# Optimization experiments

Measured on AMD Instinct MI355X. Metric: run time of the kernel, lower is better.

## Reference

```python
import jax, jax.numpy as jnp
import numpy as np

N = 50000          # nodes
E = 800000         # edges
F_IN = 128         # in_channels
C = 64             # cell channels
NCELLS = 2
STEPS = 4
MULT = 4
N_EDGE_SLOTS = 14  # 2+3+4+5 mixed-op edges per cell
N_OPS = 8          # switch_on
NUM_CLASSES = 40
BN_EPS = 1e-5
GCNII_ALPHA = 0.1


def setup_inputs() -> dict:
    key = jax.random.key(0)
    ks = jax.random.split(key, 20)
    def w(k, shape, fan_in):
        return jax.random.normal(k, shape, dtype=jnp.float32) / np.float32(np.sqrt(fan_in))
    return {
        "x": jax.random.normal(ks[0], (N, F_IN), dtype=jnp.float32),
        "edge_index": jax.random.randint(ks[1], (2, E), 0, N, dtype=jnp.int32),
        "alphas": 0.001 * jax.random.normal(ks[2], (N_EDGE_SLOTS, N_OPS), dtype=jnp.float32),
        "stem_W": w(ks[3], (F_IN, 3 * C), F_IN),
        "pre_W": w(ks[4], (F_IN, C), F_IN),
        "pre0_W0": w(ks[5], (3 * C, C), 3 * C),
        "pre1_W0": w(ks[6], (3 * C, C), 3 * C),
        "pre0_W1": w(ks[7], (3 * C, C), 3 * C),
        "pre1_W1": w(ks[8], (MULT * C, C), MULT * C),
        "W_gcn": w(ks[9], (NCELLS, N_EDGE_SLOTS, C, C), C),
        "W_sage_self": w(ks[10], (NCELLS, N_EDGE_SLOTS, C, C), C),
        "W_sage_nei": w(ks[11], (NCELLS, N_EDGE_SLOTS, C, C), C),
        "W_gin": w(ks[12], (NCELLS, N_EDGE_SLOTS, C, C), C),
        "W_gc1": w(ks[13], (NCELLS, N_EDGE_SLOTS, C, C), C),
        "W_gc2": w(ks[14], (NCELLS, N_EDGE_SLOTS, C, C), C),
        "W_mlp": w(ks[15], (NCELLS, N_EDGE_SLOTS, C, C), C),
        "W_gcnii": w(ks[16], (NCELLS, N_EDGE_SLOTS, C, C), C),
        "cls_W": w(ks[17], (MULT * C + 1, NUM_CLASSES), MULT * C + 1),
        "cls_b": jnp.zeros((NUM_CLASSES,), dtype=jnp.float32),
    }


def reference(x, edge_index, alphas, stem_W, pre_W, pre0_W0, pre1_W0, pre0_W1, pre1_W1,
              W_gcn, W_sage_self, W_sage_nei, W_gin, W_gc1, W_gc2, W_mlp, W_gcnii,
              cls_W, cls_b):
    src, dst = edge_index[0], edge_index[1]
    deg = jax.ops.segment_sum(jnp.ones((E,), jnp.float32), dst, num_segments=N)
    deg = jnp.maximum(deg, 1.0)
    inv_deg = 1.0 / deg
    inv_sqrt = jax.lax.rsqrt(deg)
    edge_norm = (inv_sqrt[src] * inv_sqrt[dst])[:, None]  # [E,1] sym-normalized coeff

    def bn(h):  # batch norm over node axis, no affine (gamma=1, beta=0)
        m = jnp.mean(h, axis=0)
        v = jnp.var(h, axis=0)
        return (h - m) * jax.lax.rsqrt(v + BN_EPS)

    def mlp(xx, W, act):  # Linear(no bias) -> BN -> optional ReLU
        h = bn(xx @ W)
        return jnp.maximum(h, 0.0) if act else h

    relu = lambda t: jnp.maximum(t, 0.0)

    def mixed_op(h, wv, ci, ej, x0):
        # shared message-passing aggregations of h over edge_index
        msg = h[src]                                             # [E,C] gather
        s_sum = jax.ops.segment_sum(msg, dst, num_segments=N)    # sum agg
        s_mean = s_sum * inv_deg[:, None]                        # mean agg
        s_norm = jax.ops.segment_sum(msg * edge_norm, dst, num_segments=N)  # gcn agg
        out = wv[1] * h                                          # skip_connect (wv[0]: none)
        out = out + wv[2] * relu(s_norm @ W_gcn[ci, ej])
        out = out + wv[3] * (h @ W_sage_self[ci, ej] + s_mean @ W_sage_nei[ci, ej])
        out = out + wv[4] * relu((h + s_sum) @ W_gin[ci, ej])
        out = out + wv[5] * (h @ W_gc1[ci, ej] + s_sum @ W_gc2[ci, ej])
        out = out + wv[6] * relu(h @ W_mlp[ci, ej])
        out = out + wv[7] * relu(((1.0 - GCNII_ALPHA) * s_norm + GCNII_ALPHA * x0) @ W_gcnii[ci, ej])
        return out

    wmix = jax.nn.softmax(alphas, axis=-1)  # [14,8], identical across cells

    s0 = s1 = mlp(x, stem_W, act=False)     # stem: MLP([in, 3C], act=None)
    x0 = mlp(x, pre_W, act=True)            # preprocess: MLP([in, C], relu)
    pre_ws = [(pre0_W0, pre1_W0), (pre0_W1, pre1_W1)]
    for ci in range(NCELLS):
        p0, p1 = pre_ws[ci]
        a = mlp(s0, p0, act=True)
        b = mlp(s1, p1, act=True)
        states = [a, b]
        offset = 0
        for _ in range(STEPS):
            s = None
            for j, h in enumerate(states):
                o = mixed_op(h, wmix[offset + j], ci, offset + j, x0)
                s = o if s is None else s + o
            offset += len(states)
            states.append(s)
        out_cell = jnp.concatenate(states[-MULT:], axis=1)  # [N, 4C]
        s0, s1 = s1, out_cell

    pooled = jnp.mean(s1, axis=1, keepdims=True)            # AdaptiveAvgPool1d(1) over channels
    logits = jnp.concatenate([pooled, s1], axis=1) @ cls_W + cls_b
    return logits
```

## Files before the change

### kernel.cpp

```cpp
#include <hip/hip_runtime.h>
#include <stdint.h>

typedef unsigned short u16;
typedef __attribute__((ext_vector_type(8))) short bh8;
typedef __attribute__((ext_vector_type(4))) float f4;

__device__ __forceinline__ float b2f(u16 u){ union{unsigned u; float f;} x; x.u = ((unsigned)u)<<16; return x.f; }
__device__ __forceinline__ u16 f2b(float f){ union{float f; unsigned u;} x; x.f = f; return (u16)((x.u + 0x7fffu + ((x.u>>16)&1u))>>16); }
__device__ __forceinline__ bh8 ld8(const u16* p){ return *reinterpret_cast<const bh8*>(p); }

#define NBK 512

__global__ __launch_bounds__(256) void k_hist(const int* dst, int* hist, int E){
  __shared__ int h[NBK];
  for (int i=threadIdx.x;i<NBK;i+=256) h[i]=0;
  __syncthreads();
  int stride = 256*gridDim.x;
  for (int i = blockIdx.x*256+threadIdx.x; i<E; i+=stride)
    atomicAdd(&h[dst[i]>>7], 1);
  __syncthreads();
  for (int i=threadIdx.x;i<NBK;i+=256){
    int v=h[i]; if (v) atomicAdd(&hist[i], v);
  }
}

__global__ __launch_bounds__(512) void k_scanb(const int* hist, int* bbase, int* bcursor){
  int t = threadIdx.x, lane = t&63, wv = t>>6;
  __shared__ int ws[8];
  int v = hist[t];
  int x = v;
  #pragma unroll
  for (int o=1;o<64;o<<=1){ int u=__shfl_up(x,(unsigned)o,64); if(lane>=o) x+=u; }
  if (lane==63) ws[wv]=x;
  __syncthreads();
  if (t<8){
    int s=ws[t];
    #pragma unroll
    for (int o=1;o<8;o<<=1){ int u=__shfl_up(s,(unsigned)o,8); if (t>=o) s+=u; }
    ws[t]=s;
  }
  __syncthreads();
  int base = (wv==0)?0:ws[wv-1];
  int ex = base + x - v;
  bbase[t]=ex; bcursor[t]=ex;
  if (t==511) bbase[512]=ex+v;
}

__global__ __launch_bounds__(256) void k_bucket(const int* src, const int* dst,
                                                int* bcursor, unsigned* bkt, int E, int nblk){
  __shared__ int h[NBK], base[NBK], lc[NBK];
  int per = (E + nblk - 1)/nblk;
  int e0 = blockIdx.x*per, e1 = min(E, e0+per);
  for (int i=threadIdx.x;i<NBK;i+=256){ h[i]=0; lc[i]=0; }
  __syncthreads();
  for (int e=e0+threadIdx.x; e<e1; e+=256) atomicAdd(&h[dst[e]>>7], 1);
  __syncthreads();
  for (int i=threadIdx.x;i<NBK;i+=256){
    int c=h[i]; base[i] = c ? atomicAdd(&bcursor[i], c) : 0;
  }
  __syncthreads();
  for (int e=e0+threadIdx.x; e<e1; e+=256){
    int d = dst[e];
    int b = d>>7;
    int r = atomicAdd(&lc[b], 1);
    bkt[base[b]+r] = ((unsigned)(d&127)<<25) | (unsigned)src[e];
  }
}

__global__ __launch_bounds__(128) void k_degb(const unsigned* bkt, const int* bbase,
                                              int* off, float* inv_deg, float* invs,
                                              int N, int E){
  int b = blockIdx.x, t = threadIdx.x;
  __shared__ int cnt[128];
  __shared__ int w0tot;
  cnt[t]=0;
  __syncthreads();
  int e0=bbase[b], e1=bbase[b+1];
  for (int e=e0+t; e<e1; e+=128) atomicAdd(&cnt[bkt[e]>>25], 1);
  __syncthreads();
  int v = cnt[t];
  int lane=t&63, wv=t>>6;
  int x=v;
  #pragma unroll
  for (int o=1;o<64;o<<=1){ int u=__shfl_up(x,(unsigned)o,64); if(lane>=o) x+=u; }
  if (t==63) w0tot=x;
  __syncthreads();
  int ex = x - v + (wv ? w0tot : 0);
  int node = b*128 + t;
  if (node < N){
    off[node] = e0 + ex;
    int d = (v<1)?1:v;
    float df=(float)d;
    inv_deg[node]=1.0f/df;
    invs[node]=rsqrtf(df);
  }
  if (b==0 && t==0) off[N]=E;
}

__global__ __launch_bounds__(128) void k_fillb(const unsigned* bkt, const int* bbase,
                                               const int* off, const float* invs,
                                               int2* csr, int N){
  int b = blockIdx.x, t = threadIdx.x;
  __shared__ int cur[128];
  int node = b*128 + t;
  cur[t] = (node < N) ? off[node] : 0;
  __syncthreads();
  int e0=bbase[b], e1=bbase[b+1];
  for (int e=e0+t; e<e1; e+=128){
    unsigned v = bkt[e];
    int i = (int)(v>>25);
    int s = (int)(v & 0x1FFFFFFu);
    int pos = atomicAdd(&cur[i], 1);
    csr[pos] = make_int2(s, __float_as_int(invs[s]));
  }
}

__global__ void k_softmax(const float* alphas, float* wmix){
  int t = threadIdx.x; int r = t >> 3, o = t & 7;
  if (r < 14){
    float v = alphas[r*8+o];
    float m = v;
    #pragma unroll
    for (int d=1; d<8; d<<=1) m = fmaxf(m, __shfl_xor(m, d, 8));
    float e = expf(v - m);
    float s = e;
    #pragma unroll
    for (int d=1; d<8; d<<=1) s += __shfl_xor(s, d, 8);
    wmix[r*8+o] = e / s;
  }
}

__global__ void k_f2b(const float* a, u16* b, int n){
  int i = blockIdx.x*256 + threadIdx.x;
  if (i < n) b[i] = f2b(a[i]);
}

__global__ void k_pack2d(const float* W, u16* Bp, int K, int ncol){
  int i = blockIdx.x*256 + threadIdx.x;
  if (i < K*ncol){
    int k = i / ncol, n = i - k*ncol;
    Bp[(size_t)n*K + k] = f2b(W[i]);
  }
}

struct PackArgs { const float* W[8]; const float* wmix; u16* dst; };
__global__ void k_pack_ops8(PackArgs P){
  int i = blockIdx.x*256 + threadIdx.x;
  if (i >= 28*8*4096) return;
  int slot28 = i >> 15;
  int rem = i & 32767;
  int mat = rem >> 12;
  int e = rem & 4095;
  int k = e >> 6, n = e & 63;
  const float* wm = P.wmix + (slot28 % 14)*8;
  size_t off = (size_t)slot28*4096 + e;
  float v = 0.f;
  switch(mat){
    case 0: v = wm[2]*P.W[0][off]; break;
    case 1: v = wm[3]*P.W[1][off] + wm[5]*P.W[4][off] + ((k==n) ? wm[1] : 0.f); break;
    case 2: v = wm[3]*P.W[2][off]; break;
    case 3: v = wm[4]*P.W[3][off]; break;
    case 4: v = wm[5]*P.W[5][off]; break;
    case 5: v = wm[6]*P.W[6][off]; break;
    case 6: v = 0.9f*wm[7]*P.W[7][off]; break;
    case 7: v = 0.1f*wm[7]*P.W[7][off]; break;
  }
  P.dst[(((size_t)slot28*8 + mat)<<12) + (n<<6) + (((k>>3) ^ (n&7))<<3) + (k&7)] = f2b(v);
}

__global__ void k_pack_cls(const float* W, u16* Bp){
  int i = blockIdx.x*256 + threadIdx.x;
  if (i < 48*256){
    int n = i >> 8, k = i & 255;
    float v = 0.f;
    if (n < 40) v = W[(size_t)(1+k)*40 + n] + W[n] * (1.f/256.f);
    Bp[(size_t)n*256 + k] = f2b(v);
  }
}

template<int NT>
__global__ __launch_bounds__(256) void k_gemm(const u16* A, int lda, const u16* Bp, int K,
                                              u16* Tb, int ldT, int Nn, float* S){
  __shared__ float sred[4][NT*16][2];
  int tid = threadIdx.x, wv = tid>>6, lane = tid&63, q = lane>>4, t = lane&15;
  int row0 = blockIdx.x*128 + wv*32;
  f4 acc[2][NT];
  #pragma unroll
  for (int a=0;a<2;a++)
    #pragma unroll
    for (int b=0;b<NT;b++) acc[a][b] = (f4){0.f,0.f,0.f,0.f};
  int nkb = K >> 5;
  const u16* arow0 = A + (size_t)(row0 + t)*lda + q*8;
  const u16* arow1 = arow0 + (size_t)16*lda;
  const u16* brow  = Bp + (size_t)t*K + q*8;
  for (int kb = 0; kb < nkb; ++kb){
    bh8 a0 = ld8(arow0 + kb*32);
    bh8 a1 = ld8(arow1 + kb*32);
    #pragma unroll
    for (int nt=0; nt<NT; ++nt){
      bh8 bf = ld8(brow + (size_t)nt*16*K + kb*32);
      acc[0][nt] = __builtin_amdgcn_mfma_f32_16x16x32_bf16(a0, bf, acc[0][nt], 0, 0, 0);
      acc[1][nt] = __builtin_amdgcn_mfma_f32_16x16x32_bf16(a1, bf, acc[1][nt], 0, 0, 0);
    }
  }
  #pragma unroll
  for (int nt=0;nt<NT;nt++){
    float ps = 0.f, pq = 0.f;
    #pragma unroll
    for (int rt=0;rt<2;rt++)
      #pragma unroll
      for (int r=0;r<4;r++){
        int row = row0 + rt*16 + q*4 + r;
        float v = acc[rt][nt][r];
        if (row < Nn){
          Tb[(size_t)row*ldT + nt*16 + t] = f2b(v);
          ps += v; pq += v*v;
        }
      }
    ps += __shfl_xor(ps, 16, 64); pq += __shfl_xor(pq, 16, 64);
    ps += __shfl_xor(ps, 32, 64); pq += __shfl_xor(pq, 32, 64);
    if (q == 0){ sred[wv][nt*16 + t][0] = ps; sred[wv][nt*16 + t][1] = pq; }
  }
  __syncthreads();
  if (tid < NT*16){
    float s = sred[0][tid][0] + sred[1][tid][0] + sred[2][tid][0] + sred[3][tid][0];
    float qq = sred[0][tid][1] + sred[1][tid][1] + sred[2][tid][1] + sred[3][tid][1];
    atomicAdd(&S[tid], s);
    atomicAdd(&S[256 + tid], qq);
  }
}

__global__ void k_norm(const u16* Tb, int ldT, int ncols, int Nn, const float* S,
                       u16* out, int rs_out, int relu, float invN){
  int i = blockIdx.x*256 + threadIdx.x;
  int nv = ncols >> 3;
  if (i >= Nn*nv) return;
  int r = i / nv, c8 = (i - r*nv)*8;
  bh8 tv = ld8(Tb + (size_t)r*ldT + c8);
  bh8 ov;
  #pragma unroll
  for (int u=0; u<8; ++u){
    int c = c8 + u;
    float m = S[c]*invN;
    float var = S[256+c]*invN - m*m;
    float xv = (b2f((u16)tv[u]) - m) * rsqrtf(var + 1e-5f);
    if (relu) xv = fmaxf(xv, 0.f);
    ov[u] = (short)f2b(xv);
  }
  *reinterpret_cast<bh8*>(out + (size_t)r*rs_out + c8) = ov;
}

#define ACC4(vv, ww) { \
    float c0 = __uint_as_float((vv).x << 16); \
    float c1 = __uint_as_float((vv).x & 0xffff0000u); \
    float c2 = __uint_as_float((vv).y << 16); \
    float c3 = __uint_as_float((vv).y & 0xffff0000u); \
    s0 += c0; s1 += c1; s2 += c2; s3 += c3; \
    n0 += c0*(ww); n1 += c1*(ww); n2 += c2*(ww); n3 += c3*(ww); }

template<int SHIFT>
__global__ __launch_bounds__(256) void k_aggv(const u16* h, const int* off, const int2* csr,
                                              const float* inv_sqrt, u16* out_sum, u16* out_norm, int Nn){
  int g = blockIdx.x*4 + (threadIdx.x >> 6);
  if (g >= Nn) return;
  int lane = threadIdx.x & 63;
  int sub = lane >> 4;
  int cb = (lane & 15) << 2;
  const u16* hp = h + cb;
  float s0=0.f,s1=0.f,s2=0.f,s3=0.f;
  float n0=0.f,n1=0.f,n2=0.f,n3=0.f;
  int e0 = off[g], e1 = off[g+1];
  int e = e0 + sub;
  for (; e + 4 < e1; e += 8){
    int2 cA = csr[e];
    int2 cB = csr[e+4];
    uint2 vA = *reinterpret_cast<const uint2*>(hp + (((unsigned)cA.x) << SHIFT));
    uint2 vB = *reinterpret_cast<const uint2*>(hp + (((unsigned)cB.x) << SHIFT));
    float wA = __int_as_float(cA.y), wB = __int_as_float(cB.y);
    ACC4(vA, wA)
    ACC4(vB, wB)
  }
  if (e < e1){
    int2 cA = csr[e];
    uint2 vA = *reinterpret_cast<const uint2*>(hp + (((unsigned)cA.x) << SHIFT));
    float wA = __int_as_float(cA.y);
    ACC4(vA, wA)
  }
  s0 += __shfl_xor(s0,16,64); s1 += __shfl_xor(s1,16,64);
  s2 += __shfl_xor(s2,16,64); s3 += __shfl_xor(s3,16,64);
  n0 += __shfl_xor(n0,16,64); n1 += __shfl_xor(n1,16,64);
  n2 += __shfl_xor(n2,16,64); n3 += __shfl_xor(n3,16,64);
  s0 += __shfl_xor(s0,32,64); s1 += __shfl_xor(s1,32,64);
  s2 += __shfl_xor(s2,32,64); s3 += __shfl_xor(s3,32,64);
  n0 += __shfl_xor(n0,32,64); n1 += __shfl_xor(n1,32,64);
  n2 += __shfl_xor(n2,32,64); n3 += __shfl_xor(n3,32,64);
  if (sub == 0){
    float ig = inv_sqrt[g];
    uint2 os, on;
    os.x = (uint)f2b(s0) | ((uint)f2b(s1) << 16);
    os.y = (uint)f2b(s2) | ((uint)f2b(s3) << 16);
    on.x = (uint)f2b(n0*ig) | ((uint)f2b(n1*ig) << 16);
    on.y = (uint)f2b(n2*ig) | ((uint)f2b(n3*ig) << 16);
    *reinterpret_cast<uint2*>(out_sum + (size_t)g*64 + cb) = os;
    *reinterpret_cast<uint2*>(out_norm + (size_t)g*64 + cb) = on;
  }
}

#define ACC4AB(va, vb, ww) { \
    float a0 = __uint_as_float((va).x << 16); \
    float a1 = __uint_as_float((va).x & 0xffff0000u); \
    float a2 = __uint_as_float((va).y << 16); \
    float a3 = __uint_as_float((va).y & 0xffff0000u); \
    float b0 = __uint_as_float((vb).x << 16); \
    float b1 = __uint_as_float((vb).x & 0xffff0000u); \
    float b2 = __uint_as_float((vb).y << 16); \
    float b3 = __uint_as_float((vb).y & 0xffff0000u); \
    sa0 += a0; sa1 += a1; sa2 += a2; sa3 += a3; \
    na0 += a0*(ww); na1 += a1*(ww); na2 += a2*(ww); na3 += a3*(ww); \
    sb0 += b0; sb1 += b1; sb2 += b2; sb3 += b3; \
    nb0 += b0*(ww); nb1 += b1*(ww); nb2 += b2*(ww); nb3 += b3*(ww); }

__global__ __launch_bounds__(256) void k_agg2v(const u16* ab, const int* off, const int2* csr,
                                               const float* inv_sqrt,
                                               u16* os0, u16* on0, u16* os1, u16* on1, int Nn){
  int g = blockIdx.x*4 + (threadIdx.x >> 6);
  if (g >= Nn) return;
  int lane = threadIdx.x & 63;
  int sub = lane >> 4;
  int cb = (lane & 15) << 2;
  const u16* hp = ab + cb;
  float sa0=0.f,sa1=0.f,sa2=0.f,sa3=0.f, na0=0.f,na1=0.f,na2=0.f,na3=0.f;
  float sb0=0.f,sb1=0.f,sb2=0.f,sb3=0.f, nb0=0.f,nb1=0.f,nb2=0.f,nb3=0.f;
  int e0 = off[g], e1 = off[g+1];
  int e = e0 + sub;
  for (; e + 4 < e1; e += 8){
    int2 cA = csr[e];
    int2 cB = csr[e+4];
    const u16* rpA = hp + (((unsigned)cA.x) << 7);
    const u16* rpB = hp + (((unsigned)cB.x) << 7);
    uint2 vaA = *reinterpret_cast<const uint2*>(rpA);
    uint2 vbA = *reinterpret_cast<const uint2*>(rpA + 64);
    uint2 vaB = *reinterpret_cast<const uint2*>(rpB);
    uint2 vbB = *reinterpret_cast<const uint2*>(rpB + 64);
    float wA = __int_as_float(cA.y), wB = __int_as_float(cB.y);
    ACC4AB(vaA, vbA, wA)
    ACC4AB(vaB, vbB, wB)
  }
  if (e < e1){
    int2 cA = csr[e];
    const u16* rpA = hp + (((unsigned)cA.x) << 7);
    uint2 vaA = *reinterpret_cast<const uint2*>(rpA);
    uint2 vbA = *reinterpret_cast<const uint2*>(rpA + 64);
    float wA = __int_as_float(cA.y);
    ACC4AB(vaA, vbA, wA)
  }
  #pragma unroll
  for (int m = 16; m <= 32; m <<= 1){
    sa0 += __shfl_xor(sa0,m,64); sa1 += __shfl_xor(sa1,m,64);
    sa2 += __shfl_xor(sa2,m,64); sa3 += __shfl_xor(sa3,m,64);
    na0 += __shfl_xor(na0,m,64); na1 += __shfl_xor(na1,m,64);
    na2 += __shfl_xor(na2,m,64); na3 += __shfl_xor(na3,m,64);
    sb0 += __shfl_xor(sb0,m,64); sb1 += __shfl_xor(sb1,m,64);
    sb2 += __shfl_xor(sb2,m,64); sb3 += __shfl_xor(sb3,m,64);
    nb0 += __shfl_xor(nb0,m,64); nb1 += __shfl_xor(nb1,m,64);
    nb2 += __shfl_xor(nb2,m,64); nb3 += __shfl_xor(nb3,m,64);
  }
  if (sub == 0){
    float ig = inv_sqrt[g];
    uint2 v;
    v.x = (uint)f2b(sa0) | ((uint)f2b(sa1) << 16);
    v.y = (uint)f2b(sa2) | ((uint)f2b(sa3) << 16);
    *reinterpret_cast<uint2*>(os0 + (size_t)g*64 + cb) = v;
    v.x = (uint)f2b(na0*ig) | ((uint)f2b(na1*ig) << 16);
    v.y = (uint)f2b(na2*ig) | ((uint)f2b(na3*ig) << 16);
    *reinterpret_cast<uint2*>(on0 + (size_t)g*64 + cb) = v;
    v.x = (uint)f2b(sb0) | ((uint)f2b(sb1) << 16);
    v.y = (uint)f2b(sb2) | ((uint)f2b(sb3) << 16);
    *reinterpret_cast<uint2*>(os1 + (size_t)g*64 + cb) = v;
    v.x = (uint)f2b(nb0*ig) | ((uint)f2b(nb1*ig) << 16);
    v.y = (uint)f2b(nb2*ig) | ((uint)f2b(nb3*ig) << 16);
    *reinterpret_cast<uint2*>(on1 + (size_t)g*64 + cb) = v;
  }
}

struct StepArgs {
  const u16* h[5]; const u16* asum[5]; const u16* anorm[5];
  int rs[5]; int slot[5]; int J;
  const u16* wpk; const float* inv_deg; const u16* x0;
  u16* out; int rs_out; int Nn;
};

__device__ __forceinline__ void mm8(const bh8 (&af)[2], const u16* wlds, int mat,
                                    int t, int q, f4 (&acc)[4]){
  #pragma unroll
  for (int kb=0;kb<2;kb++)
    #pragma unroll
    for (int nt=0;nt<4;nt++){
      bh8 bf = ld8(wlds + (mat<<12) + ((nt*16+t)<<6) + ((((kb<<2)|q) ^ (t&7))<<3));
      acc[nt] = __builtin_amdgcn_mfma_f32_16x16x32_bf16(af[kb], bf, acc[nt], 0, 0, 0);
    }
}

__global__ __launch_bounds__(512, 4)
void k_step(StepArgs A){
  __shared__ __align__(16) u16 wlds[8*4096];
  int tid = threadIdx.x, wv = tid>>6, lane = tid&63, q = lane>>4, t = lane&15;
  int row0 = blockIdx.x*128 + wv*16;
  int rA = row0 + t;
  int q8 = q*8;
  f4 idg = *reinterpret_cast<const f4*>(A.inv_deg + row0 + q*4);
  const u16* xp = A.x0 + (size_t)rA*64;
  bh8 fx[2];
  fx[0]=ld8(xp+q8); fx[1]=ld8(xp+32+q8);

  f4 oacc[4];
  #pragma unroll
  for (int b=0;b<4;b++) oacc[b] = (f4){0.f,0.f,0.f,0.f};

  uint4* wdst = reinterpret_cast<uint4*>(wlds);
  for (int j = 0; j < A.J; ++j){
    if (j) __syncthreads();
    const uint4* wsrc = reinterpret_cast<const uint4*>(A.wpk) + ((size_t)A.slot[j] << 12);
    #pragma unroll
    for (int i = 0; i < 8; ++i) wdst[tid + i*512] = wsrc[tid + i*512];

    const u16* h = A.h[j]; int rs = A.rs[j];
    const u16* hp = h + (size_t)rA*rs;
    const u16* sp = A.asum[j] + (size_t)rA*64;
    const u16* np = A.anorm[j] + (size_t)rA*64;
    bh8 fh[2], fs[2], fn[2];
    fh[0]=ld8(hp+q8); fh[1]=ld8(hp+32+q8);
    fs[0]=ld8(sp+q8); fs[1]=ld8(sp+32+q8);
    fn[0]=ld8(np+q8); fn[1]=ld8(np+32+q8);

    __syncthreads();

    mm8(fh, wlds, 1, t, q, oacc);
    mm8(fs, wlds, 4, t, q, oacc);
    f4 p[4];
    #pragma unroll
    for (int b=0;b<4;b++) p[b] = (f4){0.f,0.f,0.f,0.f};
    mm8(fh, wlds, 5, t, q, p);
    #pragma unroll
    for (int nt=0;nt<4;nt++)
      #pragma unroll
      for (int r=0;r<4;r++) oacc[nt][r] += fmaxf(p[nt][r], 0.f);
    #pragma unroll
    for (int b=0;b<4;b++) p[b] = (f4){0.f,0.f,0.f,0.f};
    mm8(fh, wlds, 3, t, q, p);
    mm8(fs, wlds, 3, t, q, p);
    #pragma unroll
    for (int nt=0;nt<4;nt++)
      #pragma unroll
      for (int r=0;r<4;r++) oacc[nt][r] += fmaxf(p[nt][r], 0.f);
    #pragma unroll
    for (int b=0;b<4;b++) p[b] = (f4){0.f,0.f,0.f,0.f};
    mm8(fn, wlds, 0, t, q, p);
    #pragma unroll
    for (int nt=0;nt<4;nt++)
      #pragma unroll
      for (int r=0;r<4;r++) oacc[nt][r] += fmaxf(p[nt][r], 0.f);
    #pragma unroll
    for (int b=0;b<4;b++) p[b] = (f4){0.f,0.f,0.f,0.f};
    mm8(fn, wlds, 6, t, q, p);
    mm8(fx, wlds, 7, t, q, p);
    #pragma unroll
    for (int nt=0;nt<4;nt++)
      #pragma unroll
      for (int r=0;r<4;r++) oacc[nt][r] += fmaxf(p[nt][r], 0.f);
    #pragma unroll
    for (int b=0;b<4;b++) p[b] = (f4){0.f,0.f,0.f,0.f};
    mm8(fs, wlds, 2, t, q, p);
    #pragma unroll
    for (int nt=0;nt<4;nt++)
      #pragma unroll
      for (int r=0;r<4;r++) oacc[nt][r] += idg[r]*p[nt][r];
  }

  #pragma unroll
  for (int nt=0;nt<4;nt++)
    #pragma unroll
    for (int r=0;r<4;r++){
      int rr = row0 + q*4 + r;
      if (rr < A.Nn) A.out[(size_t)rr*A.rs_out + nt*16 + t] = f2b(oacc[nt][r]);
    }
}

__global__ __launch_bounds__(256) void k_cls_mm(const u16* A, const u16* Bp,
                                                const float* bvec, float* out, int Nn){
  int tid = threadIdx.x, wv = tid>>6, lane = tid&63, q = lane>>4, t = lane&15;
  int row0 = blockIdx.x*128 + wv*32;
  f4 acc[2][3];
  #pragma unroll
  for (int a=0;a<2;a++)
    #pragma unroll
    for (int b=0;b<3;b++) acc[a][b] = (f4){0.f,0.f,0.f,0.f};
  const u16* arow0 = A + (size_t)(row0 + t)*256 + q*8;
  const u16* arow1 = arow0 + (size_t)16*256;
  const u16* brow  = Bp + (size_t)t*256 + q*8;
  #pragma unroll
  for (int kb = 0; kb < 8; ++kb){
    bh8 a0 = ld8(arow0 + kb*32);
    bh8 a1 = ld8(arow1 + kb*32);
    #pragma unroll
    for (int nt=0; nt<3; ++nt){
      bh8 bf = ld8(brow + (size_t)nt*16*256 + kb*32);
      acc[0][nt] = __builtin_amdgcn_mfma_f32_16x16x32_bf16(a0, bf, acc[0][nt], 0, 0, 0);
      acc[1][nt] = __builtin_amdgcn_mfma_f32_16x16x32_bf16(a1, bf, acc[1][nt], 0, 0, 0);
    }
  }
  #pragma unroll
  for (int rt=0;rt<2;rt++)
    #pragma unroll
    for (int nt=0;nt<3;nt++){
      int col = nt*16 + t;
      #pragma unroll
      for (int r=0;r<4;r++){
        int row = row0 + rt*16 + q*4 + r;
        if (row < Nn && col < 40) out[(size_t)row*40 + col] = acc[rt][nt][r] + bvec[col];
      }
    }
}

extern "C" void kernel_launch(void* const* d_in, const int* in_sizes, int n_in,
                              void* d_out, int out_size, void* d_ws, size_t ws_size,
                              hipStream_t stream){
  (void)n_in; (void)out_size; (void)ws_size;
  const float* x      = (const float*)d_in[0];
  const int*   ei     = (const int*)d_in[1];
  const float* alphas = (const float*)d_in[2];
  const float* stem_W = (const float*)d_in[3];
  const float* pre_W  = (const float*)d_in[4];
  const float* p00    = (const float*)d_in[5];
  const float* p10    = (const float*)d_in[6];
  const float* p01    = (const float*)d_in[7];
  const float* p11    = (const float*)d_in[8];
  const float* clsW = (const float*)d_in[17];
  const float* clsb = (const float*)d_in[18];

  int N = in_sizes[0] / 128;
  int E = in_sizes[1] / 2;
  const int* esrc = ei;
  const int* edst = ei + E;

  char* p = (char*)d_ws;
  auto carve = [&](size_t bytes) -> char* {
    char* r = p; p += (bytes + 255) & ~(size_t)255; return r;
  };
  int*   hist    = (int*)carve((size_t)NBK*4);
  int*   bbase   = (int*)carve((size_t)(NBK+1)*4);
  int*   bcursor = (int*)carve((size_t)NBK*4);
  unsigned* bkt  = (unsigned*)carve((size_t)E*4);
  int*   off     = (int*)carve((size_t)(N+1)*4);
  int2*  csr     = (int2*)carve((size_t)E*8);
  float* inv_deg = (float*)carve((size_t)N*4);
  float* invs    = (float*)carve((size_t)N*4);
  float* wmix    = (float*)carve(14*8*4);
  float* stats   = (float*)carve(512*4);
  u16* xb      = (u16*)carve((size_t)N*128*2);
  u16* stem_pk = (u16*)carve((size_t)192*128*2);
  u16* pre_pk  = (u16*)carve((size_t)64*128*2);
  u16* p00_pk  = (u16*)carve((size_t)64*192*2);
  u16* p10_pk  = (u16*)carve((size_t)64*192*2);
  u16* p01_pk  = (u16*)carve((size_t)64*192*2);
  u16* p11_pk  = (u16*)carve((size_t)64*256*2);
  u16* cls_pk  = (u16*)carve((size_t)48*256*2);
  u16* ops_pk  = (u16*)carve((size_t)28*8*4096*2);
  u16* T       = (u16*)carve((size_t)N*192*2);
  u16* stem_o  = (u16*)carve((size_t)N*192*2);
  u16* x0b     = (u16*)carve((size_t)N*64*2);
  u16* ab      = (u16*)carve((size_t)N*128*2);
  u16* oc0     = (u16*)carve((size_t)N*256*2);
  u16* oc1     = (u16*)carve((size_t)N*256*2);
  u16* agg     = (u16*)carve((size_t)5*2*N*64*2);
  carve(131072);

  auto aggS = [&](int j){ return agg + (size_t)j*2*N*64; };
  auto aggN = [&](int j){ return agg + (size_t)j*2*N*64 + (size_t)N*64; };

  int NB = (N + 127)/128;
  int gg = (N + 127)/128;
  int gstep = (N + 127)/128;
  int ag = (N + 3)/4;
  float invN = 1.0f/(float)N;

  hipMemsetAsync(hist, 0, (size_t)NBK*4, stream);
  k_hist<<<256,256,0,stream>>>(edst, hist, E);
  k_scanb<<<1,512,0,stream>>>(hist, bbase, bcursor);
  k_bucket<<<256,256,0,stream>>>(esrc, edst, bcursor, bkt, E, 256);
  k_degb<<<NB,128,0,stream>>>(bkt, bbase, off, inv_deg, invs, N, E);
  k_fillb<<<NB,128,0,stream>>>(bkt, bbase, off, invs, csr, N);

  k_softmax<<<1,128,0,stream>>>(alphas, wmix);
  k_f2b<<<(N*128+255)/256,256,0,stream>>>(x, xb, N*128);
  k_pack2d<<<(128*192+255)/256,256,0,stream>>>(stem_W, stem_pk, 128, 192);
  k_pack2d<<<(128*64+255)/256,256,0,stream>>>(pre_W, pre_pk, 128, 64);
  k_pack2d<<<(192*64+255)/256,256,0,stream>>>(p00, p00_pk, 192, 64);
  k_pack2d<<<(192*64+255)/256,256,0,stream>>>(p10, p10_pk, 192, 64);
  k_pack2d<<<(192*64+255)/256,256,0,stream>>>(p01, p01_pk, 192, 64);
  k_pack2d<<<(256*64+255)/256,256,0,stream>>>(p11, p11_pk, 256, 64);
  k_pack_cls<<<(48*256+255)/256,256,0,stream>>>(clsW, cls_pk);
  {
    PackArgs PA;
    for (int i = 0; i < 8; ++i) PA.W[i] = (const float*)d_in[9+i];
    PA.wmix = wmix; PA.dst = ops_pk;
    k_pack_ops8<<<(28*8*4096+255)/256,256,0,stream>>>(PA);
  }

  auto mlp = [&](const u16* A, int lda, const u16* Bp, int K, int ncol, u16* outb, int rs_out, int relu){
    hipMemsetAsync(stats, 0, 512*4, stream);
    if (ncol == 192)
      hipLaunchKernelGGL(HIP_KERNEL_NAME(k_gemm<12>), dim3(gg), dim3(256), 0, stream, A, lda, Bp, K, T, ncol, N, stats);
    else
      hipLaunchKernelGGL(HIP_KERNEL_NAME(k_gemm<4>), dim3(gg), dim3(256), 0, stream, A, lda, Bp, K, T, ncol, N, stats);
    k_norm<<<((N*(ncol>>3))+255)/256,256,0,stream>>>(T, ncol, ncol, N, stats, outb, rs_out, relu, invN);
  };

  mlp(xb, 128, stem_pk, 128, 192, stem_o, 192, 0);
  mlp(xb, 128, pre_pk, 128, 64, x0b, 64, 1);

  u16* ocs[2] = {oc0, oc1};
  const int slotbase[4] = {0, 2, 5, 9};
  for (int ci = 0; ci < 2; ++ci){
    const u16* s1in = (ci == 0) ? stem_o : oc0;
    int lda1 = (ci == 0) ? 192 : 256;
    int Kb   = (ci == 0) ? 192 : 256;
    const u16* pa = (ci == 0) ? p00_pk : p01_pk;
    const u16* pb = (ci == 0) ? p10_pk : p11_pk;
    mlp(stem_o, 192, pa, 192, 64, ab, 128, 1);
    mlp(s1in, lda1, pb, Kb, 64, ab + 64, 128, 1);

    u16* oc = ocs[ci];
    const u16* wpk_cell = ops_pk + (size_t)ci*14*8*4096;

    k_agg2v<<<ag,256,0,stream>>>(ab, off, csr, invs,
                                 aggS(0), aggN(0), aggS(1), aggN(1), N);

    const u16* st[5] = { ab, ab + 64, oc + 0, oc + 64, oc + 128 };
    const int strs[5] = {128, 128, 256, 256, 256};
    for (int step = 0; step < 4; ++step){
      StepArgs SA{};
      int J = step + 2;
      for (int j = 0; j < J; ++j){
        SA.h[j] = st[j]; SA.rs[j] = strs[j];
        SA.asum[j] = aggS(j); SA.anorm[j] = aggN(j);
        SA.slot[j] = slotbase[step] + j;
      }
      SA.J = J; SA.wpk = wpk_cell; SA.inv_deg = inv_deg; SA.x0 = x0b;
      SA.out = oc + (size_t)step*64; SA.rs_out = 256; SA.Nn = N;
      k_step<<<gstep,512,0,stream>>>(SA);
      if (step < 3)
        hipLaunchKernelGGL(HIP_KERNEL_NAME(k_aggv<8>), dim3(ag), dim3(256), 0, stream,
                           oc + (size_t)step*64, off, csr, invs, aggS(step+2), aggN(step+2), N);
    }
  }

  k_cls_mm<<<gg,256,0,stream>>>(oc1, cls_pk, clsb, (float*)d_out, N);
}
```

Before: 831.2 us.

## Double-buffer step weights in LDS and process two row tiles per wave

```diff
diff --git a/kernel.cpp b/kernel.cpp
--- a/kernel.cpp
+++ b/kernel.cpp
@@ -390,100 +390,149 @@
   u16* out; int rs_out; int Nn;
 };
 
-__device__ __forceinline__ void mm8(const bh8 (&af)[2], const u16* wlds, int mat,
-                                    int t, int q, f4 (&acc)[4]){
+__device__ __forceinline__ void mmP(const bh8 (&af)[2][2], const u16* wb, int mat,
+                                    int t, int q, f4 (&acc)[2][4]){
   #pragma unroll
   for (int kb=0;kb<2;kb++)
     #pragma unroll
     for (int nt=0;nt<4;nt++){
-      bh8 bf = ld8(wlds + (mat<<12) + ((nt*16+t)<<6) + ((((kb<<2)|q) ^ (t&7))<<3));
-      acc[nt] = __builtin_amdgcn_mfma_f32_16x16x32_bf16(af[kb], bf, acc[nt], 0, 0, 0);
+      bh8 bf = ld8(wb + (mat<<12) + ((nt*16+t)<<6) + ((((kb<<2)|q) ^ (t&7))<<3));
+      acc[0][nt] = __builtin_amdgcn_mfma_f32_16x16x32_bf16(af[0][kb], bf, acc[0][nt], 0, 0, 0);
+      acc[1][nt] = __builtin_amdgcn_mfma_f32_16x16x32_bf16(af[1][kb], bf, acc[1][nt], 0, 0, 0);
     }
 }
 
-__global__ __launch_bounds__(512, 4)
+__global__ __launch_bounds__(512, 2)
 void k_step(StepArgs A){
-  __shared__ __align__(16) u16 wlds[8*4096];
+  __shared__ __align__(16) u16 wlds[2][8*4096];
   int tid = threadIdx.x, wv = tid>>6, lane = tid&63, q = lane>>4, t = lane&15;
-  int row0 = blockIdx.x*128 + wv*16;
-  int rA = row0 + t;
+  int row0 = blockIdx.x*256 + wv*32;
+  int rA0 = row0 + t, rA1 = row0 + 16 + t;
   int q8 = q*8;
-  f4 idg = *reinterpret_cast<const f4*>(A.inv_deg + row0 + q*4);
-  const u16* xp = A.x0 + (size_t)rA*64;
-  bh8 fx[2];
-  fx[0]=ld8(xp+q8); fx[1]=ld8(xp+32+q8);
-
-  f4 oacc[4];
-  #pragma unroll
-  for (int b=0;b<4;b++) oacc[b] = (f4){0.f,0.f,0.f,0.f};
-
-  uint4* wdst = reinterpret_cast<uint4*>(wlds);
+  f4 idg0 = *reinterpret_cast<const f4*>(A.inv_deg + row0 + q*4);
+  f4 idg1 = *reinterpret_cast<const f4*>(A.inv_deg + row0 + 16 + q*4);
+  const u16* xp0 = A.x0 + (size_t)rA0*64;
+  const u16* xp1 = A.x0 + (size_t)rA1*64;
+  bh8 fx[2][2];
+  fx[0][0]=ld8(xp0+q8); fx[0][1]=ld8(xp0+32+q8);
+  fx[1][0]=ld8(xp1+q8); fx[1][1]=ld8(xp1+32+q8);
+
+  f4 oacc[2][4];
+  #pragma unroll
+  for (int a=0;a<2;a++)
+    #pragma unroll
+    for (int b=0;b<4;b++) oacc[a][b] = (f4){0.f,0.f,0.f,0.f};
+
+  uint4 w8[8];
+  {
+    const uint4* ws = reinterpret_cast<const uint4*>(A.wpk) + ((size_t)A.slot[0] << 12);
+    #pragma unroll
+    for (int i=0;i<8;i++) w8[i] = ws[tid + i*512];
+    uint4* wd = reinterpret_cast<uint4*>(&wlds[0][0]);
+    #pragma unroll
+    for (int i=0;i<8;i++) wd[tid + i*512] = w8[i];
+  }
+  __syncthreads();
+
   for (int j = 0; j < A.J; ++j){
-    if (j) __syncthreads();
-    const uint4* wsrc = reinterpret_cast<const uint4*>(A.wpk) + ((size_t)A.slot[j] << 12);
-    #pragma unroll
-    for (int i = 0; i < 8; ++i) wdst[tid + i*512] = wsrc[tid + i*512];
-
+    int cur = j & 1;
+    if (j+1 < A.J){
+      const uint4* ws = reinterpret_cast<const uint4*>(A.wpk) + ((size_t)A.slot[j+1] << 12);
+      #pragma unroll
+      for (int i=0;i<8;i++) w8[i] = ws[tid + i*512];
+    }
     const u16* h = A.h[j]; int rs = A.rs[j];
-    const u16* hp = h + (size_t)rA*rs;
-    const u16* sp = A.asum[j] + (size_t)rA*64;
-    const u16* np = A.anorm[j] + (size_t)rA*64;
-    bh8 fh[2], fs[2], fn[2];
-    fh[0]=ld8(hp+q8); fh[1]=ld8(hp+32+q8);
-    fs[0]=ld8(sp+q8); fs[1]=ld8(sp+32+q8);
-    fn[0]=ld8(np+q8); fn[1]=ld8(np+32+q8);
-
-    __syncthreads();
-
-    mm8(fh, wlds, 1, t, q, oacc);
-    mm8(fs, wlds, 4, t, q, oacc);
-    f4 p[4];
-    #pragma unroll
-    for (int b=0;b<4;b++) p[b] = (f4){0.f,0.f,0.f,0.f};
-    mm8(fh, wlds, 5, t, q, p);
+    const u16* sp = A.asum[j];
+    const u16* np = A.anorm[j];
+    bh8 fh[2][2], fs[2][2], fn[2][2];
+    fh[0][0]=ld8(h+(size_t)rA0*rs+q8);   fh[0][1]=ld8(h+(size_t)rA0*rs+32+q8);
+    fh[1][0]=ld8(h+(size_t)rA1*rs+q8);   fh[1][1]=ld8(h+(size_t)rA1*rs+32+q8);
+    fs[0][0]=ld8(sp+(size_t)rA0*64+q8);  fs[0][1]=ld8(sp+(size_t)rA0*64+32+q8);
+    fs[1][0]=ld8(sp+(size_t)rA1*64+q8);  fs[1][1]=ld8(sp+(size_t)rA1*64+32+q8);
+    fn[0][0]=ld8(np+(size_t)rA0*64+q8);  fn[0][1]=ld8(np+(size_t)rA0*64+32+q8);
+    fn[1][0]=ld8(np+(size_t)rA1*64+q8);  fn[1][1]=ld8(np+(size_t)rA1*64+32+q8);
+
+    const u16* wb = &wlds[cur][0];
+
+    mmP(fh, wb, 1, t, q, oacc);
+    mmP(fs, wb, 4, t, q, oacc);
+    f4 p[2][4];
+    #pragma unroll
+    for (int a=0;a<2;a++)
+      #pragma unroll
+      for (int b=0;b<4;b++) p[a][b] = (f4){0.f,0.f,0.f,0.f};
+    mmP(fh, wb, 5, t, q, p);
+    #pragma unroll
+    for (int rt=0;rt<2;rt++)
+      #pragma unroll
+      for (int nt=0;nt<4;nt++)
+        #pragma unroll
+        for (int r=0;r<4;r++) oacc[rt][nt][r] += fmaxf(p[rt][nt][r], 0.f);
+    #pragma unroll
+    for (int a=0;a<2;a++)
+      #pragma unroll
+      for (int b=0;b<4;b++) p[a][b] = (f4){0.f,0.f,0.f,0.f};
+    mmP(fh, wb, 3, t, q, p);
+    mmP(fs, wb, 3, t, q, p);
+    #pragma unroll
+    for (int rt=0;rt<2;rt++)
+      #pragma unroll
+      for (int nt=0;nt<4;nt++)
+        #pragma unroll
+        for (int r=0;r<4;r++) oacc[rt][nt][r] += fmaxf(p[rt][nt][r], 0.f);
+    #pragma unroll
+    for (int a=0;a<2;a++)
+      #pragma unroll
+      for (int b=0;b<4;b++) p[a][b] = (f4){0.f,0.f,0.f,0.f};
+    mmP(fn, wb, 0, t, q, p);
+    #pragma unroll
+    for (int rt=0;rt<2;rt++)
+      #pragma unroll
+      for (int nt=0;nt<4;nt++)
+        #pragma unroll
+        for (int r=0;r<4;r++) oacc[rt][nt][r] += fmaxf(p[rt][nt][r], 0.f);
+    #pragma unroll
+    for (int a=0;a<2;a++)
+      #pragma unroll
+      for (int b=0;b<4;b++) p[a][b] = (f4){0.f,0.f,0.f,0.f};
+    mmP(fn, wb, 6, t, q, p);
+    mmP(fx, wb, 7, t, q, p);
+    #pragma unroll
+    for (int rt=0;rt<2;rt++)
+      #pragma unroll
+      for (int nt=0;nt<4;nt++)
+        #pragma unroll
+        for (int r=0;r<4;r++) oacc[rt][nt][r] += fmaxf(p[rt][nt][r], 0.f);
+    #pragma unroll
+    for (int a=0;a<2;a++)
+      #pragma unroll
+      for (int b=0;b<4;b++) p[a][b] = (f4){0.f,0.f,0.f,0.f};
+    mmP(fs, wb, 2, t, q, p);
     #pragma unroll
     for (int nt=0;nt<4;nt++)
       #pragma unroll
-      for (int r=0;r<4;r++) oacc[nt][r] += fmaxf(p[nt][r], 0.f);
-    #pragma unroll
-    for (int b=0;b<4;b++) p[b] = (f4){0.f,0.f,0.f,0.f};
-    mm8(fh, wlds, 3, t, q, p);
-    mm8(fs, wlds, 3, t, q, p);
+      for (int r=0;r<4;r++){
+        oacc[0][nt][r] += idg0[r]*p[0][nt][r];
+        oacc[1][nt][r] += idg1[r]*p[1][nt][r];
+      }
+
+    if (j+1 < A.J){
+      uint4* wd = reinterpret_cast<uint4*>(&wlds[cur^1][0]);
+      #pragma unroll
+      for (int i=0;i<8;i++) wd[tid + i*512] = w8[i];
+      __syncthreads();
+    }
+  }
+
+  #pragma unroll
+  for (int rt=0;rt<2;rt++)
     #pragma unroll
     for (int nt=0;nt<4;nt++)
       #pragma unroll
-      for (int r=0;r<4;r++) oacc[nt][r] += fmaxf(p[nt][r], 0.f);
-    #pragma unroll
-    for (int b=0;b<4;b++) p[b] = (f4){0.f,0.f,0.f,0.f};
-    mm8(fn, wlds, 0, t, q, p);
-    #pragma unroll
-    for (int nt=0;nt<4;nt++)
-      #pragma unroll
-      for (int r=0;r<4;r++) oacc[nt][r] += fmaxf(p[nt][r], 0.f);
-    #pragma unroll
-    for (int b=0;b<4;b++) p[b] = (f4){0.f,0.f,0.f,0.f};
-    mm8(fn, wlds, 6, t, q, p);
-    mm8(fx, wlds, 7, t, q, p);
-    #pragma unroll
-    for (int nt=0;nt<4;nt++)
-      #pragma unroll
-      for (int r=0;r<4;r++) oacc[nt][r] += fmaxf(p[nt][r], 0.f);
-    #pragma unroll
-    for (int b=0;b<4;b++) p[b] = (f4){0.f,0.f,0.f,0.f};
-    mm8(fs, wlds, 2, t, q, p);
-    #pragma unroll
-    for (int nt=0;nt<4;nt++)
-      #pragma unroll
-      for (int r=0;r<4;r++) oacc[nt][r] += idg[r]*p[nt][r];
-  }
-
-  #pragma unroll
-  for (int nt=0;nt<4;nt++)
-    #pragma unroll
-    for (int r=0;r<4;r++){
-      int rr = row0 + q*4 + r;
-      if (rr < A.Nn) A.out[(size_t)rr*A.rs_out + nt*16 + t] = f2b(oacc[nt][r]);
-    }
+      for (int r=0;r<4;r++){
+        int rr = row0 + rt*16 + q*4 + r;
+        if (rr < A.Nn) A.out[(size_t)rr*A.rs_out + nt*16 + t] = f2b(oacc[rt][nt][r]);
+      }
 }
 
 __global__ __launch_bounds__(256) void k_cls_mm(const u16* A, const u16* Bp,
@@ -573,14 +622,14 @@
   u16* oc0     = (u16*)carve((size_t)N*256*2);
   u16* oc1     = (u16*)carve((size_t)N*256*2);
   u16* agg     = (u16*)carve((size_t)5*2*N*64*2);
-  carve(131072);
+  carve(262144);
 
   auto aggS = [&](int j){ return agg + (size_t)j*2*N*64; };
   auto aggN = [&](int j){ return agg + (size_t)j*2*N*64 + (size_t)N*64; };
 
   int NB = (N + 127)/128;
   int gg = (N + 127)/128;
-  int gstep = (N + 127)/128;
+  int gstep = (N + 255)/256;
   int ag = (N + 3)/4;
   float invN = 1.0f/(float)N;
 
```

Result: slower. 919.1 us (+10.6%).

## Template GEMM on K, replace stat atomics with per-block partials, async LDS weight staging

Applied to the files above, without the earlier changes.

```diff
diff --git a/kernel.cpp b/kernel.cpp
--- a/kernel.cpp
+++ b/kernel.cpp
@@ -8,6 +8,12 @@
 __device__ __forceinline__ float b2f(u16 u){ union{unsigned u; float f;} x; x.u = ((unsigned)u)<<16; return x.f; }
 __device__ __forceinline__ u16 f2b(float f){ union{float f; unsigned u;} x; x.f = f; return (u16)((x.u + 0x7fffu + ((x.u>>16)&1u))>>16); }
 __device__ __forceinline__ bh8 ld8(const u16* p){ return *reinterpret_cast<const bh8*>(p); }
+
+__device__ __forceinline__ void gld16(const void* g, void* l){
+  __builtin_amdgcn_global_load_lds(
+    (const __attribute__((address_space(1))) void*)g,
+    (__attribute__((address_space(3))) void*)l, 16, 0, 0);
+}
 
 #define NBK 512
 
@@ -178,9 +184,11 @@
   }
 }
 
-template<int NT>
-__global__ __launch_bounds__(256) void k_gemm(const u16* A, int lda, const u16* Bp, int K,
-                                              u16* Tb, int ldT, int Nn, float* S){
+template<int NT, int NKB>
+__global__ __launch_bounds__(256) void k_gemm(const u16* A, const u16* Bp,
+                                              u16* Tb, int Nn, float* Sp){
+  const int K = NKB*32;
+  const int ldT = NT*16;
   __shared__ float sred[4][NT*16][2];
   int tid = threadIdx.x, wv = tid>>6, lane = tid&63, q = lane>>4, t = lane&15;
   int row0 = blockIdx.x*128 + wv*32;
@@ -189,11 +197,11 @@
   for (int a=0;a<2;a++)
     #pragma unroll
     for (int b=0;b<NT;b++) acc[a][b] = (f4){0.f,0.f,0.f,0.f};
-  int nkb = K >> 5;
-  const u16* arow0 = A + (size_t)(row0 + t)*lda + q*8;
-  const u16* arow1 = arow0 + (size_t)16*lda;
+  const u16* arow0 = A + (size_t)(row0 + t)*K + q*8;
+  const u16* arow1 = arow0 + (size_t)16*K;
   const u16* brow  = Bp + (size_t)t*K + q*8;
-  for (int kb = 0; kb < nkb; ++kb){
+  #pragma unroll
+  for (int kb = 0; kb < NKB; ++kb){
     bh8 a0 = ld8(arow0 + kb*32);
     bh8 a1 = ld8(arow1 + kb*32);
     #pragma unroll
@@ -225,8 +233,24 @@
   if (tid < NT*16){
     float s = sred[0][tid][0] + sred[1][tid][0] + sred[2][tid][0] + sred[3][tid][0];
     float qq = sred[0][tid][1] + sred[1][tid][1] + sred[2][tid][1] + sred[3][tid][1];
-    atomicAdd(&S[tid], s);
-    atomicAdd(&S[256 + tid], qq);
+    float* sp = Sp + (size_t)blockIdx.x*(2*NT*16);
+    sp[tid] = s;
+    sp[NT*16 + tid] = qq;
+  }
+}
+
+__global__ __launch_bounds__(256) void k_redstats(const float* Sp, float* S, int ncol, int nb){
+  int c2 = blockIdx.x*4 + (threadIdx.x>>6);
+  int lane = threadIdx.x & 63;
+  if (c2 >= 2*ncol) return;
+  int stride = 2*ncol;
+  float s = 0.f;
+  for (int b = lane; b < nb; b += 64) s += Sp[(size_t)b*stride + c2];
+  #pragma unroll
+  for (int m=1; m<64; m<<=1) s += __shfl_xor(s, m, 64);
+  if (lane == 0){
+    int c = (c2 < ncol) ? c2 : (256 + (c2 - ncol));
+    S[c] = s;
   }
 }
 
@@ -401,7 +425,7 @@
     }
 }
 
-__global__ __launch_bounds__(512, 4)
+__global__ __launch_bounds__(512)
 void k_step(StepArgs A){
   __shared__ __align__(16) u16 wlds[8*4096];
   int tid = threadIdx.x, wv = tid>>6, lane = tid&63, q = lane>>4, t = lane&15;
@@ -417,18 +441,24 @@
   #pragma unroll
   for (int b=0;b<4;b++) oacc[b] = (f4){0.f,0.f,0.f,0.f};
 
-  uint4* wdst = reinterpret_cast<uint4*>(wlds);
+  auto stage = [&](int slot){
+    const u16* wg = A.wpk + ((size_t)slot << 15);
+    #pragma unroll
+    for (int i=0;i<8;i++){
+      int cbase = i*512 + wv*64;
+      gld16(wg + (size_t)(cbase + lane)*8, &wlds[(size_t)cbase*8]);
+    }
+  };
+
   for (int j = 0; j < A.J; ++j){
     if (j) __syncthreads();
-    const uint4* wsrc = reinterpret_cast<const uint4*>(A.wpk) + ((size_t)A.slot[j] << 12);
-    #pragma unroll
-    for (int i = 0; i < 8; ++i) wdst[tid + i*512] = wsrc[tid + i*512];
+    stage(A.slot[j]);
 
     const u16* h = A.h[j]; int rs = A.rs[j];
     const u16* hp = h + (size_t)rA*rs;
     const u16* sp = A.asum[j] + (size_t)rA*64;
     const u16* np = A.anorm[j] + (size_t)rA*64;
-    bh8 fh[2], fs[2], fn[2];
+    bh8 fh[2], fs[2], fn[2], ax[2];
     fh[0]=ld8(hp+q8); fh[1]=ld8(hp+32+q8);
     fs[0]=ld8(sp+q8); fs[1]=ld8(sp+32+q8);
     fn[0]=ld8(np+q8); fn[1]=ld8(np+32+q8);
@@ -475,6 +505,7 @@
     for (int nt=0;nt<4;nt++)
       #pragma unroll
       for (int r=0;r<4;r++) oacc[nt][r] += idg[r]*p[nt][r];
+    (void)ax;
   }
 
   #pragma unroll
@@ -557,6 +588,7 @@
   float* invs    = (float*)carve((size_t)N*4);
   float* wmix    = (float*)carve(14*8*4);
   float* stats   = (float*)carve(512*4);
+  float* Sp      = (float*)carve((size_t)512*384*4);
   u16* xb      = (u16*)carve((size_t)N*128*2);
   u16* stem_pk = (u16*)carve((size_t)192*128*2);
   u16* pre_pk  = (u16*)carve((size_t)64*128*2);
@@ -573,7 +605,7 @@
   u16* oc0     = (u16*)carve((size_t)N*256*2);
   u16* oc1     = (u16*)carve((size_t)N*256*2);
   u16* agg     = (u16*)carve((size_t)5*2*N*64*2);
-  carve(131072);
+  carve(262144);
 
   auto aggS = [&](int j){ return agg + (size_t)j*2*N*64; };
   auto aggN = [&](int j){ return agg + (size_t)j*2*N*64 + (size_t)N*64; };
@@ -607,28 +639,31 @@
     k_pack_ops8<<<(28*8*4096+255)/256,256,0,stream>>>(PA);
   }
 
-  auto mlp = [&](const u16* A, int lda, const u16* Bp, int K, int ncol, u16* outb, int rs_out, int relu){
-    hipMemsetAsync(stats, 0, 512*4, stream);
+  auto mlp = [&](const u16* A, int K, const u16* Bp, int ncol, u16* outb, int rs_out, int relu){
     if (ncol == 192)
-      hipLaunchKernelGGL(HIP_KERNEL_NAME(k_gemm<12>), dim3(gg), dim3(256), 0, stream, A, lda, Bp, K, T, ncol, N, stats);
+      hipLaunchKernelGGL(HIP_KERNEL_NAME(k_gemm<12,4>), dim3(gg), dim3(256), 0, stream, A, Bp, T, N, Sp);
+    else if (K == 128)
+      hipLaunchKernelGGL(HIP_KERNEL_NAME(k_gemm<4,4>), dim3(gg), dim3(256), 0, stream, A, Bp, T, N, Sp);
+    else if (K == 192)
+      hipLaunchKernelGGL(HIP_KERNEL_NAME(k_gemm<4,6>), dim3(gg), dim3(256), 0, stream, A, Bp, T, N, Sp);
     else
-      hipLaunchKernelGGL(HIP_KERNEL_NAME(k_gemm<4>), dim3(gg), dim3(256), 0, stream, A, lda, Bp, K, T, ncol, N, stats);
+      hipLaunchKernelGGL(HIP_KERNEL_NAME(k_gemm<4,8>), dim3(gg), dim3(256), 0, stream, A, Bp, T, N, Sp);
+    k_redstats<<<(2*ncol+3)/4,256,0,stream>>>(Sp, stats, ncol, gg);
     k_norm<<<((N*(ncol>>3))+255)/256,256,0,stream>>>(T, ncol, ncol, N, stats, outb, rs_out, relu, invN);
   };
 
-  mlp(xb, 128, stem_pk, 128, 192, stem_o, 192, 0);
-  mlp(xb, 128, pre_pk, 128, 64, x0b, 64, 1);
+  mlp(xb, 128, stem_pk, 192, stem_o, 192, 0);
+  mlp(xb, 128, pre_pk, 64, x0b, 64, 1);
 
   u16* ocs[2] = {oc0, oc1};
   const int slotbase[4] = {0, 2, 5, 9};
   for (int ci = 0; ci < 2; ++ci){
     const u16* s1in = (ci == 0) ? stem_o : oc0;
-    int lda1 = (ci == 0) ? 192 : 256;
     int Kb   = (ci == 0) ? 192 : 256;
     const u16* pa = (ci == 0) ? p00_pk : p01_pk;
     const u16* pb = (ci == 0) ? p10_pk : p11_pk;
-    mlp(stem_o, 192, pa, 192, 64, ab, 128, 1);
-    mlp(s1in, lda1, pb, Kb, 64, ab + 64, 128, 1);
+    mlp(stem_o, 192, pa, 64, ab, 128, 1);
+    mlp(s1in, Kb, pb, 64, ab + 64, 128, 1);
 
     u16* oc = ocs[ci];
     const u16* wpk_cell = ops_pk + (size_t)ci*14*8*4096;
```

New measurement: 831.3 us. Within noise of the previous version (+0.0%).
